# Kernel optimization log

Hardware: AMD Instinct MI355X
Metric: run time of the kernel (lower is better)

Reference implementation:

```python
import jax, jax.numpy as jnp
import numpy as np

N_NODES = 100000
N_EDGES = 1600000
NFEAT = 64
NHID = 64
NCLASS = 16


def setup_inputs() -> dict:
    key = jax.random.key(0)
    k_x, k_e, k_w1, k_b1, k_w2, k_b2 = jax.random.split(key, 6)
    x = jax.random.normal(k_x, (N_NODES, NFEAT), dtype=jnp.float32)
    edge_index = jax.random.randint(k_e, (2, N_EDGES), 0, N_NODES, dtype=jnp.int64)
    # Glorot-ish init for the GIN update MLP
    W1 = jax.random.normal(k_w1, (NFEAT, NHID), dtype=jnp.float32) * (1.0 / np.sqrt(NFEAT))
    b1 = jnp.zeros((NHID,), dtype=jnp.float32)
    W2 = jax.random.normal(k_w2, (NHID, NCLASS), dtype=jnp.float32) * (1.0 / np.sqrt(NHID))
    b2 = jnp.zeros((NCLASS,), dtype=jnp.float32)
    eps = jnp.float32(0.0)  # train_eps=True, initialized to 0
    return {"x": x, "edge_index": edge_index, "eps": eps,
            "W1": W1, "b1": b1, "W2": W2, "b2": b2}


def reference(x, edge_index, eps, W1, b1, W2, b2):
    # GINConv: out = MLP((1 + eps) * x + sum_{j in N(i)} x_j)
    src = edge_index[0]  # message source nodes
    dst = edge_index[1]  # aggregation targets (source_to_target flow)
    agg = jax.ops.segment_sum(x[src], dst, num_segments=x.shape[0])  # [N, F]
    h = (1.0 + eps) * x + agg
    # MLP([nfeat, nhid, nclass]): Linear -> ReLU -> (dropout=identity in eval) -> Linear
    h = jax.nn.relu(h @ W1 + b1)
    return h @ W2 + b2
```

## Files before the change

### kernel.cpp

```cpp
#include <hip/hip_runtime.h>
#include <hip/hip_bf16.h>
#include <hip/hip_fp16.h>


#define NFEAT 64
#define NHID 64
#define NCLASS 16

#define PCAP 6144
#define MAXBUCK 512
#define PT 512
#define PEPT 8
#define ST 1024
#define SEPT 6

__global__ __launch_bounds__(512) void k_init(int* __restrict__ cursor, int nbuck)
{
    int t = threadIdx.x;
    if (t < nbuck) cursor[t] = t * PCAP;
}

__global__ __launch_bounds__(512) void k_cvt(
    const float4* __restrict__ x4, uint2* __restrict__ xh, int n4)
{
    int i = blockIdx.x * 512 + threadIdx.x;
    if (i < n4) {
        float4 v = x4[i];
        __half2 a = __floats2half2_rn(v.x, v.y);
        __half2 b = __floats2half2_rn(v.z, v.w);
        uint2 o;
        o.x = *reinterpret_cast<unsigned int*>(&a);
        o.y = *reinterpret_cast<unsigned int*>(&b);
        xh[i] = o;
    }
}

__global__ __launch_bounds__(PT) void k_part(
    const int* __restrict__ ei, int* __restrict__ cursor,
    int* __restrict__ dsts, int n_edges, int nbuck)
{
    __shared__ int lcnt[MAXBUCK];
    __shared__ int sbase[MAXBUCK];
    int tid = threadIdx.x;
    for (int i = tid; i < nbuck; i += PT) lcnt[i] = 0;
    __syncthreads();

    int e0 = blockIdx.x * (PT * PEPT);
    int bk[PEPT], rk[PEPT], pk[PEPT];
    #pragma unroll
    for (int k = 0; k < PEPT; ++k) {
        int e = e0 + k * PT + tid;
        if (e < n_edges) {
            int src = ei[e];
            int dst = ei[n_edges + e];
            int b = dst >> 8;
            bk[k] = b;
            pk[k] = (src << 8) | (dst & 255);
            rk[k] = atomicAdd(&lcnt[b], 1);
        } else bk[k] = -1;
    }
    __syncthreads();
    for (int i = tid; i < nbuck; i += PT)
        sbase[i] = lcnt[i] ? atomicAdd(&cursor[i], lcnt[i]) : 0;
    __syncthreads();
    #pragma unroll
    for (int k = 0; k < PEPT; ++k)
        if (bk[k] >= 0) dsts[sbase[bk[k]] + rk[k]] = pk[k];
}

__global__ __launch_bounds__(512) void k_bscan(
    const int* __restrict__ cursor, int* __restrict__ bbase,
    int* __restrict__ row_ptr, int nbuck, int n_edges, int n_nodes)
{
    __shared__ int sw[8];
    int t = threadIdx.x, lane = t & 63, wid = t >> 6;
    int v = (t < nbuck) ? (cursor[t] - t * PCAP) : 0;
    int s = v;
    #pragma unroll
    for (int off = 1; off < 64; off <<= 1) {
        int u = __shfl_up(s, off);
        if (lane >= off) s += u;
    }
    if (lane == 63) sw[wid] = s;
    __syncthreads();
    if (t == 0) { int a = 0; for (int i = 0; i < 8; ++i) { int tmp = sw[i]; sw[i] = a; a += tmp; } }
    __syncthreads();
    if (t < nbuck) bbase[t] = (s - v) + sw[wid];
    if (t == 0) row_ptr[n_nodes] = n_edges;
}

__global__ __launch_bounds__(ST) void k_bsort(
    const int* __restrict__ dsts, const int* __restrict__ cursor,
    const int* __restrict__ bbase, int* __restrict__ csr_src,
    int* __restrict__ row_ptr, int n_nodes)
{
    __shared__ int cnt[256];
    __shared__ int off[256];
    int b = blockIdx.x;
    int tid = threadIdx.x, lane = tid & 63, wid = tid >> 6;
    int s = cursor[b] - b * PCAP;
    int gin = b * PCAP;
    if (tid < 256) cnt[tid] = 0;
    __syncthreads();

    int dk[SEPT], rk[SEPT], sk[SEPT];
    #pragma unroll
    for (int k = 0; k < SEPT; ++k) {
        int i = k * ST + tid;
        if (i < s) {
            int p = dsts[gin + i];
            int d = p & 255;
            dk[k] = d;
            sk[k] = p >> 8;
            rk[k] = atomicAdd(&cnt[d], 1);
        } else dk[k] = -1;
    }
    __syncthreads();
    if (wid == 0) {
        int c0 = cnt[lane * 4], c1 = cnt[lane * 4 + 1], c2 = cnt[lane * 4 + 2], c3 = cnt[lane * 4 + 3];
        int p1 = c0, p2 = p1 + c1, p3 = p2 + c2, p4 = p3 + c3;
        int ss = p4;
        #pragma unroll
        for (int o = 1; o < 64; o <<= 1) {
            int u = __shfl_up(ss, o);
            if (lane >= o) ss += u;
        }
        int base = ss - p4;
        off[lane * 4] = base; off[lane * 4 + 1] = base + p1;
        off[lane * 4 + 2] = base + p2; off[lane * 4 + 3] = base + p3;
    }
    __syncthreads();
    int bb = bbase[b];
    #pragma unroll
    for (int k = 0; k < SEPT; ++k)
        if (dk[k] >= 0) csr_src[bb + off[dk[k]] + rk[k]] = sk[k];
    int node = b * 256 + tid;
    if (tid < 256 && node < n_nodes) row_ptr[node] = bb + off[tid];
}

__global__ __launch_bounds__(512) void k_gather_mlp(
    const float4* __restrict__ x4,
    const uint2* __restrict__ xh,
    const int* __restrict__ row_ptr,
    const int* __restrict__ csr_src,
    const float* __restrict__ eps_p,
    const float* __restrict__ W1,
    const float* __restrict__ b1,
    const float* __restrict__ W2,
    const float* __restrict__ b2,
    float* __restrict__ out,
    int n_nodes)
{
    __shared__ float sW1[NFEAT * NHID];
    __shared__ float sW2[NHID * 17];
    __shared__ float sb1[NHID];
    __shared__ float sb2[NCLASS];
    __shared__ float sh0[32][68];
    __shared__ float sh1[32][68];
    __shared__ int   sIdx[8][64];

    int tid = threadIdx.x;
    for (int i = tid; i < NFEAT * NHID; i += 512) sW1[i] = W1[i];
    for (int i = tid; i < NHID * NCLASS; i += 512) sW2[(i >> 4) * 17 + (i & 15)] = W2[i];
    if (tid < NHID) sb1[tid] = b1[tid];
    if (tid < NCLASS) sb2[tid] = b2[tid];
    __syncthreads();

    float eps1 = 1.0f + eps_p[0];
    int wave = tid >> 6;
    int lane = tid & 63;
    int q = lane >> 4;
    int f = lane & 15;
    int s8 = (lane >> 3) & 1;
    int f8 = lane & 7;
    int nloc = wave * 4 + q;

    for (int nb0 = blockIdx.x * 32; nb0 < n_nodes; nb0 += gridDim.x * 32) {
        int myNode = nb0 + nloc;
        bool valid = myNode < n_nodes;
        int s = 0, e = 0;
        if (valid) { s = row_ptr[myNode]; e = row_ptr[myNode + 1]; }
        int dmax = e - s;
        dmax = max(dmax, __shfl_xor(dmax, 16));
        dmax = max(dmax, __shfl_xor(dmax, 32));

        float4 accA = make_float4(0.f, 0.f, 0.f, 0.f);
        float4 accB = make_float4(0.f, 0.f, 0.f, 0.f);
        for (int base = 0; base < dmax; base += 16) {
            int p = s + base + f;
            sIdx[wave][lane] = (p < e) ? csr_src[p] : -1;
            #pragma unroll
            for (int t = 0; t < 8; ++t) {
                int idx = sIdx[wave][q * 16 + t * 2 + s8];
                if (idx >= 0) {
                    const uint4* rp = (const uint4*)(xh + (size_t)idx * 16);
                    uint4 u = rp[f8];
                    __half2 h0 = *reinterpret_cast<__half2*>(&u.x);
                    __half2 h1 = *reinterpret_cast<__half2*>(&u.y);
                    __half2 h2 = *reinterpret_cast<__half2*>(&u.z);
                    __half2 h3 = *reinterpret_cast<__half2*>(&u.w);
                    float2 g0 = __half22float2(h0);
                    float2 g1 = __half22float2(h1);
                    float2 g2 = __half22float2(h2);
                    float2 g3 = __half22float2(h3);
                    accA.x += g0.x; accA.y += g0.y; accA.z += g1.x; accA.w += g1.y;
                    accB.x += g2.x; accB.y += g2.y; accB.z += g3.x; accB.w += g3.y;
                }
            }
        }
        accA.x += __shfl_xor(accA.x, 8); accA.y += __shfl_xor(accA.y, 8);
        accA.z += __shfl_xor(accA.z, 8); accA.w += __shfl_xor(accA.w, 8);
        accB.x += __shfl_xor(accB.x, 8); accB.y += __shfl_xor(accB.y, 8);
        accB.z += __shfl_xor(accB.z, 8); accB.w += __shfl_xor(accB.w, 8);
        if (s8 == 0) {
            if (valid) {
                float4 xa = x4[(size_t)myNode * 16 + f8 * 2];
                float4 xb = x4[(size_t)myNode * 16 + f8 * 2 + 1];
                accA.x += eps1 * xa.x; accA.y += eps1 * xa.y;
                accA.z += eps1 * xa.z; accA.w += eps1 * xa.w;
                accB.x += eps1 * xb.x; accB.y += eps1 * xb.y;
                accB.z += eps1 * xb.z; accB.w += eps1 * xb.w;
            }
            *(float4*)&sh0[nloc][f8 * 8] = accA;
            *(float4*)&sh0[nloc][f8 * 8 + 4] = accB;
        }

        int r = wave * 4;
        float a0 = sb1[lane], a1 = a0, a2 = a0, a3 = a0;
        #pragma unroll
        for (int kk = 0; kk < 16; ++kk) {
            float4 h0 = *(const float4*)&sh0[r + 0][kk * 4];
            float4 h1v = *(const float4*)&sh0[r + 1][kk * 4];
            float4 h2 = *(const float4*)&sh0[r + 2][kk * 4];
            float4 h3 = *(const float4*)&sh0[r + 3][kk * 4];
            #pragma unroll
            for (int i = 0; i < 4; ++i) {
                float w = sW1[(kk * 4 + i) * NHID + lane];
                a0 += ((const float*)&h0)[i] * w;
                a1 += ((const float*)&h1v)[i] * w;
                a2 += ((const float*)&h2)[i] * w;
                a3 += ((const float*)&h3)[i] * w;
            }
        }
        sh1[r + 0][lane] = fmaxf(a0, 0.f);
        sh1[r + 1][lane] = fmaxf(a1, 0.f);
        sh1[r + 2][lane] = fmaxf(a2, 0.f);
        sh1[r + 3][lane] = fmaxf(a3, 0.f);

        float o = sb2[f];
        #pragma unroll
        for (int jj = 0; jj < 16; ++jj) {
            float4 hv = *(const float4*)&sh1[nloc][jj * 4];
            o += hv.x * sW2[(jj * 4 + 0) * 17 + f];
            o += hv.y * sW2[(jj * 4 + 1) * 17 + f];
            o += hv.z * sW2[(jj * 4 + 2) * 17 + f];
            o += hv.w * sW2[(jj * 4 + 3) * 17 + f];
        }
        if (valid) out[(size_t)myNode * NCLASS + f] = o;
    }
}

extern "C" void kernel_launch(void* const* d_in, const int* in_sizes, int n_in,
                              void* d_out, int out_size, void* d_ws, size_t ws_size,
                              hipStream_t stream) {
    const float* x   = (const float*)d_in[0];
    const int*   ei  = (const int*)d_in[1];
    const float* eps = (const float*)d_in[2];
    const float* W1  = (const float*)d_in[3];
    const float* b1  = (const float*)d_in[4];
    const float* W2  = (const float*)d_in[5];
    const float* b2  = (const float*)d_in[6];
    float* out = (float*)d_out;

    int n_nodes = in_sizes[0] / NFEAT;
    int n_edges = in_sizes[1] / 2;
    int nbuck = (n_nodes + 255) / 256;

    char* ws = (char*)d_ws;
    int* cursor  = (int*)ws;
    int* bbase   = (int*)(ws + 2048);
    int* dsts    = (int*)(ws + 4096);
    size_t o_rp  = 4096 + (size_t)nbuck * PCAP * 4;
    int* row_ptr = (int*)(ws + o_rp);
    int* csr_src = (int*)(ws + o_rp + 400128);
    size_t o_xh  = o_rp + 400128 + (size_t)n_edges * 4;
    o_xh = (o_xh + 15) & ~(size_t)15;
    uint2* xh    = (uint2*)(ws + o_xh);

    int n4 = n_nodes * 16;
    k_init<<<1, 512, 0, stream>>>(cursor, nbuck);
    k_cvt<<<(n4 + 511) / 512, 512, 0, stream>>>((const float4*)x, xh, n4);
    k_part<<<(n_edges + PT * PEPT - 1) / (PT * PEPT), PT, 0, stream>>>(
        ei, cursor, dsts, n_edges, nbuck);
    k_bscan<<<1, 512, 0, stream>>>(cursor, bbase, row_ptr, nbuck, n_edges, n_nodes);
    k_bsort<<<nbuck, ST, 0, stream>>>(dsts, cursor, bbase, csr_src, row_ptr, n_nodes);
    int ntile = (n_nodes + 31) / 32;
    int ngrid = ntile < 1024 ? ntile : 1024;
    k_gather_mlp<<<ngrid, 512, 0, stream>>>(
        (const float4*)x, xh, row_ptr, csr_src, eps, W1, b1, W2, b2, out, n_nodes);
}
```

Baseline: 185.5 us.

## Fuse CSR build stages into one cooperative kernel with grid syncs

Merges the init, fp16 conversion, edge partition, bucket scan and bucket sort kernels into a single cooperative kernel. Each stage is separated by a grid-wide sync instead of a separate launch. The aim is to remove per-launch overhead and the idle gaps between the small preprocessing kernels. In exchange, the sort phase drops from 1024 to 512 threads per block, each handling twice as many elements, and grid syncs add their own cost. The partition phase only covers every edge if the bucket-count grid happens to span all of them.

```diff
diff --git a/kernel.cpp b/kernel.cpp
--- a/kernel.cpp
+++ b/kernel.cpp
@@ -1,6 +1,9 @@
 #include <hip/hip_runtime.h>
 #include <hip/hip_bf16.h>
 #include <hip/hip_fp16.h>
+#include <hip/hip_cooperative_groups.h>
+
+namespace cg = cooperative_groups;
 
 
 #define NFEAT 64
@@ -9,22 +12,27 @@
 
 #define PCAP 6144
 #define MAXBUCK 512
-#define PT 512
+#define BT 512
 #define PEPT 8
-#define ST 1024
-#define SEPT 6
-
-__global__ __launch_bounds__(512) void k_init(int* __restrict__ cursor, int nbuck)
+#define SEPT2 12
+
+__global__ __launch_bounds__(BT) void k_build(
+    const float4* __restrict__ x4, uint2* __restrict__ xh,
+    const int* __restrict__ ei,
+    int* __restrict__ cursor, int* __restrict__ bbase,
+    int* __restrict__ dsts, int* __restrict__ csr_src,
+    int* __restrict__ row_ptr,
+    int n_nodes, int n_edges, int nbuck, int n4)
 {
-    int t = threadIdx.x;
-    if (t < nbuck) cursor[t] = t * PCAP;
-}
-
-__global__ __launch_bounds__(512) void k_cvt(
-    const float4* __restrict__ x4, uint2* __restrict__ xh, int n4)
-{
-    int i = blockIdx.x * 512 + threadIdx.x;
-    if (i < n4) {
+    __shared__ int lcnt[MAXBUCK];
+    __shared__ int sbase[MAXBUCK];
+    __shared__ int sw[8];
+    cg::grid_group grid = cg::this_grid();
+    int tid = threadIdx.x;
+    int bid = blockIdx.x;
+    int lane = tid & 63, wid = tid >> 6;
+
+    for (int i = bid * BT + tid; i < n4; i += gridDim.x * BT) {
         float4 v = x4[i];
         __half2 a = __floats2half2_rn(v.x, v.y);
         __half2 b = __floats2half2_rn(v.z, v.w);
@@ -33,109 +41,94 @@
         o.y = *reinterpret_cast<unsigned int*>(&b);
         xh[i] = o;
     }
-}
-
-__global__ __launch_bounds__(PT) void k_part(
-    const int* __restrict__ ei, int* __restrict__ cursor,
-    int* __restrict__ dsts, int n_edges, int nbuck)
-{
-    __shared__ int lcnt[MAXBUCK];
-    __shared__ int sbase[MAXBUCK];
-    int tid = threadIdx.x;
-    for (int i = tid; i < nbuck; i += PT) lcnt[i] = 0;
-    __syncthreads();
-
-    int e0 = blockIdx.x * (PT * PEPT);
-    int bk[PEPT], rk[PEPT], pk[PEPT];
-    #pragma unroll
-    for (int k = 0; k < PEPT; ++k) {
-        int e = e0 + k * PT + tid;
-        if (e < n_edges) {
-            int src = ei[e];
-            int dst = ei[n_edges + e];
-            int b = dst >> 8;
-            bk[k] = b;
-            pk[k] = (src << 8) | (dst & 255);
-            rk[k] = atomicAdd(&lcnt[b], 1);
-        } else bk[k] = -1;
-    }
-    __syncthreads();
-    for (int i = tid; i < nbuck; i += PT)
-        sbase[i] = lcnt[i] ? atomicAdd(&cursor[i], lcnt[i]) : 0;
-    __syncthreads();
-    #pragma unroll
-    for (int k = 0; k < PEPT; ++k)
-        if (bk[k] >= 0) dsts[sbase[bk[k]] + rk[k]] = pk[k];
-}
-
-__global__ __launch_bounds__(512) void k_bscan(
-    const int* __restrict__ cursor, int* __restrict__ bbase,
-    int* __restrict__ row_ptr, int nbuck, int n_edges, int n_nodes)
-{
-    __shared__ int sw[8];
-    int t = threadIdx.x, lane = t & 63, wid = t >> 6;
-    int v = (t < nbuck) ? (cursor[t] - t * PCAP) : 0;
-    int s = v;
-    #pragma unroll
-    for (int off = 1; off < 64; off <<= 1) {
-        int u = __shfl_up(s, off);
-        if (lane >= off) s += u;
-    }
-    if (lane == 63) sw[wid] = s;
-    __syncthreads();
-    if (t == 0) { int a = 0; for (int i = 0; i < 8; ++i) { int tmp = sw[i]; sw[i] = a; a += tmp; } }
-    __syncthreads();
-    if (t < nbuck) bbase[t] = (s - v) + sw[wid];
-    if (t == 0) row_ptr[n_nodes] = n_edges;
-}
-
-__global__ __launch_bounds__(ST) void k_bsort(
-    const int* __restrict__ dsts, const int* __restrict__ cursor,
-    const int* __restrict__ bbase, int* __restrict__ csr_src,
-    int* __restrict__ row_ptr, int n_nodes)
-{
-    __shared__ int cnt[256];
-    __shared__ int off[256];
-    int b = blockIdx.x;
-    int tid = threadIdx.x, lane = tid & 63, wid = tid >> 6;
-    int s = cursor[b] - b * PCAP;
-    int gin = b * PCAP;
-    if (tid < 256) cnt[tid] = 0;
-    __syncthreads();
-
-    int dk[SEPT], rk[SEPT], sk[SEPT];
-    #pragma unroll
-    for (int k = 0; k < SEPT; ++k) {
-        int i = k * ST + tid;
-        if (i < s) {
-            int p = dsts[gin + i];
-            int d = p & 255;
-            dk[k] = d;
-            sk[k] = p >> 8;
-            rk[k] = atomicAdd(&cnt[d], 1);
-        } else dk[k] = -1;
-    }
-    __syncthreads();
-    if (wid == 0) {
-        int c0 = cnt[lane * 4], c1 = cnt[lane * 4 + 1], c2 = cnt[lane * 4 + 2], c3 = cnt[lane * 4 + 3];
-        int p1 = c0, p2 = p1 + c1, p3 = p2 + c2, p4 = p3 + c3;
-        int ss = p4;
-        #pragma unroll
-        for (int o = 1; o < 64; o <<= 1) {
-            int u = __shfl_up(ss, o);
-            if (lane >= o) ss += u;
-        }
-        int base = ss - p4;
-        off[lane * 4] = base; off[lane * 4 + 1] = base + p1;
-        off[lane * 4 + 2] = base + p2; off[lane * 4 + 3] = base + p3;
-    }
-    __syncthreads();
-    int bb = bbase[b];
-    #pragma unroll
-    for (int k = 0; k < SEPT; ++k)
-        if (dk[k] >= 0) csr_src[bb + off[dk[k]] + rk[k]] = sk[k];
-    int node = b * 256 + tid;
-    if (tid < 256 && node < n_nodes) row_ptr[node] = bb + off[tid];
+    if (bid == 0 && tid < nbuck) cursor[tid] = tid * PCAP;
+    grid.sync();
+
+    {
+        for (int i = tid; i < nbuck; i += BT) lcnt[i] = 0;
+        __syncthreads();
+        int e0 = bid * (BT * PEPT);
+        int bk[PEPT], rk[PEPT], pk[PEPT];
+        #pragma unroll
+        for (int k = 0; k < PEPT; ++k) {
+            int e = e0 + k * BT + tid;
+            if (e < n_edges) {
+                int src = ei[e];
+                int dst = ei[n_edges + e];
+                int b = dst >> 8;
+                bk[k] = b;
+                pk[k] = (src << 8) | (dst & 255);
+                rk[k] = atomicAdd(&lcnt[b], 1);
+            } else bk[k] = -1;
+        }
+        __syncthreads();
+        for (int i = tid; i < nbuck; i += BT)
+            sbase[i] = lcnt[i] ? atomicAdd(&cursor[i], lcnt[i]) : 0;
+        __syncthreads();
+        #pragma unroll
+        for (int k = 0; k < PEPT; ++k)
+            if (bk[k] >= 0) dsts[sbase[bk[k]] + rk[k]] = pk[k];
+    }
+    grid.sync();
+
+    if (bid == 0) {
+        int v = (tid < nbuck) ? (cursor[tid] - tid * PCAP) : 0;
+        int s = v;
+        #pragma unroll
+        for (int off = 1; off < 64; off <<= 1) {
+            int u = __shfl_up(s, off);
+            if (lane >= off) s += u;
+        }
+        if (lane == 63) sw[wid] = s;
+        __syncthreads();
+        if (tid == 0) { int a = 0; for (int i = 0; i < 8; ++i) { int tmp = sw[i]; sw[i] = a; a += tmp; } }
+        __syncthreads();
+        if (tid < nbuck) bbase[tid] = (s - v) + sw[wid];
+        if (tid == 0) row_ptr[n_nodes] = n_edges;
+    }
+    grid.sync();
+
+    {
+        int b = bid;
+        int s = cursor[b] - b * PCAP;
+        int gin = b * PCAP;
+        if (tid < 256) lcnt[tid] = 0;
+        __syncthreads();
+
+        int dk[SEPT2], rk[SEPT2], sk[SEPT2];
+        #pragma unroll
+        for (int k = 0; k < SEPT2; ++k) {
+            int i = k * BT + tid;
+            if (i < s) {
+                int p = dsts[gin + i];
+                int d = p & 255;
+                dk[k] = d;
+                sk[k] = p >> 8;
+                rk[k] = atomicAdd(&lcnt[d], 1);
+            } else dk[k] = -1;
+        }
+        __syncthreads();
+        if (wid == 0) {
+            int c0 = lcnt[lane * 4], c1 = lcnt[lane * 4 + 1], c2 = lcnt[lane * 4 + 2], c3 = lcnt[lane * 4 + 3];
+            int p1 = c0, p2 = p1 + c1, p3 = p2 + c2, p4 = p3 + c3;
+            int ss = p4;
+            #pragma unroll
+            for (int o = 1; o < 64; o <<= 1) {
+                int u = __shfl_up(ss, o);
+                if (lane >= o) ss += u;
+            }
+            int base = ss - p4;
+            sbase[lane * 4] = base; sbase[lane * 4 + 1] = base + p1;
+            sbase[lane * 4 + 2] = base + p2; sbase[lane * 4 + 3] = base + p3;
+        }
+        __syncthreads();
+        int bb = bbase[b];
+        #pragma unroll
+        for (int k = 0; k < SEPT2; ++k)
+            if (dk[k] >= 0) csr_src[bb + sbase[dk[k]] + rk[k]] = sk[k];
+        int node = b * 256 + tid;
+        if (tid < 256 && node < n_nodes) row_ptr[node] = bb + sbase[tid];
+    }
 }
 
 __global__ __launch_bounds__(512) void k_gather_mlp(
@@ -288,12 +281,17 @@
     uint2* xh    = (uint2*)(ws + o_xh);
 
     int n4 = n_nodes * 16;
-    k_init<<<1, 512, 0, stream>>>(cursor, nbuck);
-    k_cvt<<<(n4 + 511) / 512, 512, 0, stream>>>((const float4*)x, xh, n4);
-    k_part<<<(n_edges + PT * PEPT - 1) / (PT * PEPT), PT, 0, stream>>>(
-        ei, cursor, dsts, n_edges, nbuck);
-    k_bscan<<<1, 512, 0, stream>>>(cursor, bbase, row_ptr, nbuck, n_edges, n_nodes);
-    k_bsort<<<nbuck, ST, 0, stream>>>(dsts, cursor, bbase, csr_src, row_ptr, n_nodes);
+
+    const float4* x4c = (const float4*)x;
+    uint2* xhp = xh;
+    const int* eip = ei;
+    int* cursorp = cursor; int* bbasep = bbase; int* dstsp = dsts;
+    int* csrp = csr_src; int* rpp = row_ptr;
+    void* bargs[] = { &x4c, &xhp, &eip, &cursorp, &bbasep, &dstsp, &csrp, &rpp,
+                      &n_nodes, &n_edges, &nbuck, &n4 };
+    hipLaunchCooperativeKernel((void*)k_build, dim3(nbuck), dim3(BT),
+                               bargs, 0, stream);
+
     int ntile = (n_nodes + 31) / 32;
     int ngrid = ntile < 1024 ? ntile : 1024;
     k_gather_mlp<<<ngrid, 512, 0, stream>>>(
```

After: 348.6 us. 1.88x slower.

## Drop bucket scan and init kernels using padded CSR with start/end arrays

Applied to the files above, without the earlier changes.

Folds cursor initialization into the conversion kernel and removes the single-block bucket prefix-scan kernel. Each bucket now writes its CSR segment at a fixed padded offset (b*PCAP), and per-node start and end indices are stored separately instead of a compact row_ptr. This cuts two kernel launches and a serial dependency, at the cost of a sparser csr_src layout, an extra row_end array, and a hard dependence on no bucket exceeding PCAP.

```diff
diff --git a/kernel.cpp b/kernel.cpp
--- a/kernel.cpp
+++ b/kernel.cpp
@@ -14,14 +14,9 @@
 #define ST 1024
 #define SEPT 6
 
-__global__ __launch_bounds__(512) void k_init(int* __restrict__ cursor, int nbuck)
-{
-    int t = threadIdx.x;
-    if (t < nbuck) cursor[t] = t * PCAP;
-}
-
 __global__ __launch_bounds__(512) void k_cvt(
-    const float4* __restrict__ x4, uint2* __restrict__ xh, int n4)
+    const float4* __restrict__ x4, uint2* __restrict__ xh,
+    int* __restrict__ cursor, int n4, int nbuck)
 {
     int i = blockIdx.x * 512 + threadIdx.x;
     if (i < n4) {
@@ -33,6 +28,8 @@
         o.y = *reinterpret_cast<unsigned int*>(&b);
         xh[i] = o;
     }
+    if (blockIdx.x == 0 && threadIdx.x < nbuck)
+        cursor[threadIdx.x] = threadIdx.x * PCAP;
 }
 
 __global__ __launch_bounds__(PT) void k_part(
@@ -68,31 +65,10 @@
         if (bk[k] >= 0) dsts[sbase[bk[k]] + rk[k]] = pk[k];
 }
 
-__global__ __launch_bounds__(512) void k_bscan(
-    const int* __restrict__ cursor, int* __restrict__ bbase,
-    int* __restrict__ row_ptr, int nbuck, int n_edges, int n_nodes)
-{
-    __shared__ int sw[8];
-    int t = threadIdx.x, lane = t & 63, wid = t >> 6;
-    int v = (t < nbuck) ? (cursor[t] - t * PCAP) : 0;
-    int s = v;
-    #pragma unroll
-    for (int off = 1; off < 64; off <<= 1) {
-        int u = __shfl_up(s, off);
-        if (lane >= off) s += u;
-    }
-    if (lane == 63) sw[wid] = s;
-    __syncthreads();
-    if (t == 0) { int a = 0; for (int i = 0; i < 8; ++i) { int tmp = sw[i]; sw[i] = a; a += tmp; } }
-    __syncthreads();
-    if (t < nbuck) bbase[t] = (s - v) + sw[wid];
-    if (t == 0) row_ptr[n_nodes] = n_edges;
-}
-
 __global__ __launch_bounds__(ST) void k_bsort(
     const int* __restrict__ dsts, const int* __restrict__ cursor,
-    const int* __restrict__ bbase, int* __restrict__ csr_src,
-    int* __restrict__ row_ptr, int n_nodes)
+    int* __restrict__ csr_src,
+    int* __restrict__ row_start, int* __restrict__ row_end, int n_nodes)
 {
     __shared__ int cnt[256];
     __shared__ int off[256];
@@ -130,18 +106,22 @@
         off[lane * 4 + 2] = base + p2; off[lane * 4 + 3] = base + p3;
     }
     __syncthreads();
-    int bb = bbase[b];
+    int bb = b * PCAP;
     #pragma unroll
     for (int k = 0; k < SEPT; ++k)
         if (dk[k] >= 0) csr_src[bb + off[dk[k]] + rk[k]] = sk[k];
     int node = b * 256 + tid;
-    if (tid < 256 && node < n_nodes) row_ptr[node] = bb + off[tid];
+    if (tid < 256 && node < n_nodes) {
+        row_start[node] = bb + off[tid];
+        row_end[node]   = bb + off[tid] + cnt[tid];
+    }
 }
 
 __global__ __launch_bounds__(512) void k_gather_mlp(
     const float4* __restrict__ x4,
     const uint2* __restrict__ xh,
-    const int* __restrict__ row_ptr,
+    const int* __restrict__ row_start,
+    const int* __restrict__ row_end,
     const int* __restrict__ csr_src,
     const float* __restrict__ eps_p,
     const float* __restrict__ W1,
@@ -179,7 +159,7 @@
         int myNode = nb0 + nloc;
         bool valid = myNode < n_nodes;
         int s = 0, e = 0;
-        if (valid) { s = row_ptr[myNode]; e = row_ptr[myNode + 1]; }
+        if (valid) { s = row_start[myNode]; e = row_end[myNode]; }
         int dmax = e - s;
         dmax = max(dmax, __shfl_xor(dmax, 16));
         dmax = max(dmax, __shfl_xor(dmax, 32));
@@ -277,25 +257,23 @@
     int nbuck = (n_nodes + 255) / 256;
 
     char* ws = (char*)d_ws;
-    int* cursor  = (int*)ws;
-    int* bbase   = (int*)(ws + 2048);
-    int* dsts    = (int*)(ws + 4096);
-    size_t o_rp  = 4096 + (size_t)nbuck * PCAP * 4;
-    int* row_ptr = (int*)(ws + o_rp);
-    int* csr_src = (int*)(ws + o_rp + 400128);
-    size_t o_xh  = o_rp + 400128 + (size_t)n_edges * 4;
+    int* cursor    = (int*)ws;
+    int* dsts      = (int*)(ws + 4096);
+    size_t o_rs    = 4096 + (size_t)nbuck * PCAP * 4;
+    int* row_start = (int*)(ws + o_rs);
+    int* row_end   = (int*)(ws + o_rs + 400128);
+    int* csr_src   = (int*)(ws + o_rs + 800256);
+    size_t o_xh    = o_rs + 800256 + (size_t)nbuck * PCAP * 4;
     o_xh = (o_xh + 15) & ~(size_t)15;
-    uint2* xh    = (uint2*)(ws + o_xh);
+    uint2* xh      = (uint2*)(ws + o_xh);
 
     int n4 = n_nodes * 16;
-    k_init<<<1, 512, 0, stream>>>(cursor, nbuck);
-    k_cvt<<<(n4 + 511) / 512, 512, 0, stream>>>((const float4*)x, xh, n4);
+    k_cvt<<<(n4 + 511) / 512, 512, 0, stream>>>((const float4*)x, xh, cursor, n4, nbuck);
     k_part<<<(n_edges + PT * PEPT - 1) / (PT * PEPT), PT, 0, stream>>>(
         ei, cursor, dsts, n_edges, nbuck);
-    k_bscan<<<1, 512, 0, stream>>>(cursor, bbase, row_ptr, nbuck, n_edges, n_nodes);
-    k_bsort<<<nbuck, ST, 0, stream>>>(dsts, cursor, bbase, csr_src, row_ptr, n_nodes);
+    k_bsort<<<nbuck, ST, 0, stream>>>(dsts, cursor, csr_src, row_start, row_end, n_nodes);
     int ntile = (n_nodes + 31) / 32;
     int ngrid = ntile < 1024 ? ntile : 1024;
     k_gather_mlp<<<ngrid, 512, 0, stream>>>(
-        (const float4*)x, xh, row_ptr, csr_src, eps, W1, b1, W2, b2, out, n_nodes);
-}
+        (const float4*)x, xh, row_start, row_end, csr_src, eps, W1, b1, W2, b2, out, n_nodes);
+}
```

After: 183.6 us. No clear change (-1.0%).
